# Optimization experiments

Measured on AMD Instinct MI355X. Metric: run time of the kernel, lower is better.

Reference implementation:

```python
import jax, jax.numpy as jnp
import numpy as np

B, S, D, H = 4, 2048, 512, 8

def setup_inputs() -> dict:
    key = jax.random.key(0)
    ks = jax.random.split(key, 6)
    query = jax.random.normal(ks[0], (B, S, D), dtype=jnp.float32)
    value = jax.random.normal(ks[1], (B, S, D), dtype=jnp.float32)
    # causal additive mask, broadcast over heads: [H, S, S]
    causal = jnp.where(jnp.tril(jnp.ones((S, S), dtype=bool)), 0.0, -1e9).astype(jnp.float32)
    mask = jnp.broadcast_to(causal[None, :, :], (H, S, S))
    sd = 1.0 / np.sqrt(D)
    Wq = jax.random.normal(ks[2], (D, D), dtype=jnp.float32) * sd
    Wkv = jax.random.normal(ks[3], (D, 2 * D), dtype=jnp.float32) * sd
    Wo = jax.random.normal(ks[4], (D, D), dtype=jnp.float32) * sd
    normalizer = jnp.asarray(1.0 / np.sqrt(D // H), dtype=jnp.float32)  # 1/sqrt(head_size)
    head_mults = jnp.ones((1, 1, H, 1), dtype=jnp.float32)
    return {"query": query, "value": value, "mask": mask, "Wq": Wq, "Wkv": Wkv,
            "Wo": Wo, "normalizer": normalizer, "head_mults": head_mults}

def reference(query, value, mask, Wq, Wkv, Wo, normalizer, head_mults):
    b, sq, d = query.shape
    h = head_mults.shape[2]
    q = (query @ Wq).reshape(b, sq, h, -1)                 # [b,q,h,hd]
    k, v = jnp.split(value @ Wkv, 2, axis=-1)
    sk = value.shape[1]
    k = k.reshape(b, sk, h, -1)
    v = v.reshape(b, sk, h, -1)
    score = jnp.einsum('bqhd,bkhd->bhqk', q, k) * normalizer
    score = score + mask[None, :, :, :]
    align = jax.nn.softmax(score, axis=-1)
    heads = jnp.einsum('bhqk,bkhd->bqhd', align, v)        # [b,q,h,hd]
    # cross-head normalization (over head axis, ddof=0 like tf.reduce_std)
    mean = jnp.mean(heads, axis=-2, keepdims=True)
    std = jnp.std(heads, axis=-2, keepdims=True)
    heads = (heads - mean) / (std + 0.01)
    heads = heads * head_mults
    out = heads.reshape(b, sq, d) @ Wo
    return out
```

## Files before the change

kernel.cpp:

```cpp
#include <hip/hip_runtime.h>


typedef float  f32x4  __attribute__((ext_vector_type(4)));
typedef __bf16 bf16x8 __attribute__((ext_vector_type(8)));
typedef short  s16x4  __attribute__((ext_vector_type(4)));
typedef unsigned short u16;

#define BS 2048
#define DD 512
#define NH 8
#define NQ (4 * BS * DD)

__device__ __forceinline__ u16 f2bf(float f) {
  union { float f; unsigned u; } v; v.f = f;
  unsigned r = v.u + 0x7fffu + ((v.u >> 16) & 1u);
  return (u16)(r >> 16);
}
__device__ __forceinline__ float bf2f(u16 b) {
  union { unsigned u; float f; } v; v.u = ((unsigned)b) << 16; return v.f;
}

__device__ __forceinline__ void gll16(const u16* g, u16* l) {
  __builtin_amdgcn_global_load_lds((const __attribute__((address_space(1))) void*)g,
                                   (__attribute__((address_space(3))) void*)l, 16, 0, 0);
}

#if defined(__has_builtin)
#if __has_builtin(__builtin_amdgcn_mfma_f32_16x16x16bf16_1k)
#define HAVE_1K 1
#endif
#endif
__device__ __forceinline__ f32x4 mfma_pv(s16x4 a, s16x4 b, f32x4 c) {
#ifdef HAVE_1K
  return __builtin_amdgcn_mfma_f32_16x16x16bf16_1k(a, b, c, 0, 0, 0);
#else
  bf16x8 a8 = {}, b8 = {};
  *(s16x4*)&a8 = a; *(s16x4*)&b8 = b;
  return __builtin_amdgcn_mfma_f32_16x16x32_bf16(a8, b8, c, 0, 0, 0);
#endif
}

__global__ __launch_bounds__(256) void prep(const float* __restrict__ q,
                                            const float* __restrict__ v,
                                            const float* __restrict__ Wq,
                                            const float* __restrict__ Wkv,
                                            const float* __restrict__ Wo,
                                            u16* __restrict__ qb, u16* __restrict__ vb,
                                            u16* __restrict__ WqT, u16* __restrict__ WkvT,
                                            u16* __restrict__ WoT) {
  __shared__ float Ts[64][65];
  const int t = threadIdx.x;
  int bx = blockIdx.x;
  if (bx < 8192) {
    int i = (bx * 256 + t) * 4;
    const float* s; u16* d;
    if (i < NQ) { s = q + i; d = qb + i; }
    else        { s = v + (i - NQ); d = vb + (i - NQ); }
    float4 x = *(const float4*)s;
    ushort4 o; o.x = f2bf(x.x); o.y = f2bf(x.y); o.z = f2bf(x.z); o.w = f2bf(x.w);
    *(ushort4*)d = o;
    return;
  }
  int tb = bx - 8192;
  const float* W; u16* Wt; int N, ntn;
  if (tb < 64)       { W = Wq;  Wt = WqT;  N = 512;  ntn = 8; }
  else if (tb < 192) { W = Wkv; Wt = WkvT; N = 1024; ntn = 16; tb -= 64; }
  else               { W = Wo;  Wt = WoT;  N = 512;  ntn = 8;  tb -= 192; }
  int tk = tb / ntn, tn = tb - tk * ntn;
  int r = t >> 2, c0 = (t & 3) * 16;
  const float* src = &W[(long)(tk * 64 + r) * N + tn * 64 + c0];
#pragma unroll
  for (int j = 0; j < 4; ++j) {
    float4 x = *(const float4*)(src + j * 4);
    Ts[r][c0 + j * 4 + 0] = x.x; Ts[r][c0 + j * 4 + 1] = x.y;
    Ts[r][c0 + j * 4 + 2] = x.z; Ts[r][c0 + j * 4 + 3] = x.w;
  }
  __syncthreads();
  u16* dst = &Wt[(long)(tn * 64 + r) * 512 + tk * 64 + c0];
#pragma unroll
  for (int m = 0; m < 4; ++m) {
    ushort4 o;
    o.x = f2bf(Ts[c0 + m * 4 + 0][r]); o.y = f2bf(Ts[c0 + m * 4 + 1][r]);
    o.z = f2bf(Ts[c0 + m * 4 + 2][r]); o.w = f2bf(Ts[c0 + m * 4 + 3][r]);
    *(ushort4*)(dst + m * 4) = o;
  }
}

__device__ __forceinline__ void gemm_core(const u16* __restrict__ A,
                                          const u16* __restrict__ Bt,
                                          int m0, int n0, int K,
                                          u16* Al, u16* Bl, f32x4 acc[4][4]) {
  const int t = threadIdx.x;
  const int wv = t >> 6, ln = t & 63, qd = ln >> 4, l16 = ln & 15;
  const int rw = (wv & 1) * 64, cw = (wv >> 1) * 64;
  const int sr = wv * 16 + (ln >> 2), sc = (ln & 3) * 8;
  for (int k0 = 0; k0 < K; k0 += 32) {
    __syncthreads();
#pragma unroll
    for (int c = 0; c < 2; ++c) {
      int r = c * 64 + sr;
      gll16(&A[(long)(m0 + r) * K + k0 + sc], &Al[r * 32 + sc]);
      gll16(&Bt[(long)(n0 + r) * K + k0 + sc], &Bl[r * 32 + sc]);
    }
    __syncthreads();
    bf16x8 af[4], bfr[4];
#pragma unroll
    for (int i = 0; i < 4; ++i) af[i] = *(const bf16x8*)&Al[(rw + i * 16 + l16) * 32 + qd * 8];
#pragma unroll
    for (int j = 0; j < 4; ++j) bfr[j] = *(const bf16x8*)&Bl[(cw + j * 16 + l16) * 32 + qd * 8];
#pragma unroll
    for (int i = 0; i < 4; ++i)
#pragma unroll
      for (int j = 0; j < 4; ++j)
        acc[i][j] = __builtin_amdgcn_mfma_f32_16x16x32_bf16(af[i], bfr[j], acc[i][j], 0, 0, 0);
  }
}

__global__ __launch_bounds__(256) void qkv_gemm(const u16* __restrict__ qA,
                                                const u16* __restrict__ vA,
                                                const u16* __restrict__ WqT,
                                                const u16* __restrict__ WkvT,
                                                u16* __restrict__ Qb,
                                                u16* __restrict__ Kb,
                                                u16* __restrict__ Vt) {
  __shared__ __align__(16) u16 Al[128 * 32];
  __shared__ __align__(16) u16 Bl[128 * 32];
  const bool isQ = blockIdx.y < 4;
  const u16* A = isQ ? qA : vA;
  const u16* Bt = isQ ? WqT : WkvT;
  const int n0 = (isQ ? blockIdx.y : blockIdx.y - 4) * 128;
  const int m0 = blockIdx.x * 128;
  f32x4 acc[4][4] = {};
  gemm_core(A, Bt, m0, n0, 512, Al, Bl, acc);
  const int t = threadIdx.x;
  const int wv = t >> 6, ln = t & 63, qd = ln >> 4, l16 = ln & 15;
  const int rw = (wv & 1) * 64, cw = (wv >> 1) * 64;
  if (isQ) {
#pragma unroll
    for (int i = 0; i < 4; ++i)
#pragma unroll
      for (int j = 0; j < 4; ++j) {
        int row = m0 + rw + i * 16 + qd * 4, col = n0 + cw + j * 16 + l16;
#pragma unroll
        for (int r = 0; r < 4; ++r)
          Qb[(long)(row + r) * 512 + col] = f2bf(acc[i][j][r]);
      }
  } else {
#pragma unroll
    for (int j = 0; j < 4; ++j) {
      int col = n0 + cw + j * 16 + l16;
      if (col < 512) {
#pragma unroll
        for (int i = 0; i < 4; ++i) {
          int row = m0 + rw + i * 16 + qd * 4;
#pragma unroll
          for (int r = 0; r < 4; ++r)
            Kb[(long)(row + r) * 512 + col] = f2bf(acc[i][j][r]);
        }
      } else {
        int c2 = col - 512, hh = c2 >> 6, dd = c2 & 63;
#pragma unroll
        for (int i = 0; i < 4; ++i) {
          int sg = m0 + rw + i * 16 + qd * 4;
          int bb = sg >> 11, ss = sg & 2047;
          ushort4 o;
          o.x = f2bf(acc[i][j][0]); o.y = f2bf(acc[i][j][1]);
          o.z = f2bf(acc[i][j][2]); o.w = f2bf(acc[i][j][3]);
          *(ushort4*)&Vt[((long)(bb * 8 + hh) * 64 + dd) * 2048 + ss] = o;
        }
      }
    }
  }
}

__global__ __launch_bounds__(256) void out_gemm(const u16* __restrict__ A,
                                                const u16* __restrict__ Bt,
                                                float* __restrict__ C) {
  __shared__ __align__(16) u16 Al[128 * 32];
  __shared__ __align__(16) u16 Bl[128 * 32];
  const int m0 = blockIdx.x * 128, n0 = blockIdx.y * 128;
  f32x4 acc[4][4] = {};
  gemm_core(A, Bt, m0, n0, 512, Al, Bl, acc);
  const int t = threadIdx.x;
  const int wv = t >> 6, ln = t & 63, qd = ln >> 4, l16 = ln & 15;
  const int rw = (wv & 1) * 64, cw = (wv >> 1) * 64;
#pragma unroll
  for (int i = 0; i < 4; ++i)
#pragma unroll
    for (int j = 0; j < 4; ++j) {
      int row = m0 + rw + i * 16 + qd * 4, col = n0 + cw + j * 16 + l16;
#pragma unroll
      for (int r = 0; r < 4; ++r)
        C[(long)(row + r) * 512 + col] = acc[i][j][r];
    }
}

__global__ __launch_bounds__(256) void attn(const u16* __restrict__ Qb,
                                            const u16* __restrict__ Kb,
                                            const u16* __restrict__ Vt,
                                            u16* __restrict__ heads,
                                            const float* __restrict__ normp) {
  constexpr int ST = 72;
  __shared__ __align__(16) u16 Qs[64 * ST], Ks[64 * ST], Vts[64 * ST];
  const float scale2 = normp[0] * 1.44269504f;
  const int t = threadIdx.x;
  const int wv = t >> 6, ln = t & 63, qd = ln >> 4, l16 = ln & 15;
  const int sr = t >> 2, scg = (t & 3) * 16;
  const int h = blockIdx.y, b = blockIdx.z;
  const int bs0 = b * BS;
  const u16* vtb = Vt + ((long)(b * 8 + h) * 64) * 2048;

  for (int qsel = 0; qsel < 2; ++qsel) {
    const int qt = qsel ? (31 - (int)blockIdx.x) : (int)blockIdx.x;
    __syncthreads();
    {
      const u16* src = &Qb[(long)(bs0 + qt * 64 + sr) * 512 + h * 64 + scg];
      *(bf16x8*)&Qs[sr * ST + scg] = *(const bf16x8*)src;
      *(bf16x8*)&Qs[sr * ST + scg + 8] = *(const bf16x8*)(src + 8);
    }
    bf16x8 kr0, kr1, vr0, vr1;
#define FETCH(KB) do { \
      const u16* kp_ = &Kb[(long)(bs0 + (KB) * 64 + sr) * 512 + h * 64 + scg]; \
      kr0 = *(const bf16x8*)kp_; kr1 = *(const bf16x8*)(kp_ + 8); \
      const u16* vp_ = &vtb[(long)sr * 2048 + (KB) * 64 + scg]; \
      vr0 = *(const bf16x8*)vp_; vr1 = *(const bf16x8*)(vp_ + 8); } while (0)
    FETCH(0);
    float m_i = -1e30f, l_i = 0.f;
    f32x4 o[4] = {};

    for (int kb = 0; kb <= qt; ++kb) {
      __syncthreads();
      *(bf16x8*)&Ks[sr * ST + scg] = kr0;
      *(bf16x8*)&Ks[sr * ST + scg + 8] = kr1;
      *(bf16x8*)&Vts[sr * ST + scg] = vr0;
      *(bf16x8*)&Vts[sr * ST + scg + 8] = vr1;
      __syncthreads();
      if (kb < qt) FETCH(kb + 1);

      f32x4 s[4] = {};
#pragma unroll
      for (int c = 0; c < 2; ++c) {
        bf16x8 bq = *(const bf16x8*)&Qs[(wv * 16 + l16) * ST + c * 32 + qd * 8];
#pragma unroll
        for (int nt = 0; nt < 4; ++nt) {
          bf16x8 ak = *(const bf16x8*)&Ks[(nt * 16 + l16) * ST + c * 32 + qd * 8];
          s[nt] = __builtin_amdgcn_mfma_f32_16x16x32_bf16(ak, bq, s[nt], 0, 0, 0);
        }
      }

      const int limi = (kb == qt) ? (wv * 16 + l16) : 1 << 20;
      float mx = -1e30f;
#pragma unroll
      for (int nt = 0; nt < 4; ++nt)
#pragma unroll
        for (int r = 0; r < 4; ++r) {
          float v = s[nt][r] * scale2;
          if (nt * 16 + qd * 4 + r > limi) v = -1e30f;
          s[nt][r] = v;
          mx = fmaxf(mx, v);
        }
      mx = fmaxf(mx, __shfl_xor(mx, 16));
      mx = fmaxf(mx, __shfl_xor(mx, 32));
      float mn = fmaxf(m_i, mx);
      float al = exp2f(m_i - mn);
      float rs = 0.f;
#pragma unroll
      for (int nt = 0; nt < 4; ++nt)
#pragma unroll
        for (int r = 0; r < 4; ++r) {
          float p = exp2f(s[nt][r] - mn);
          s[nt][r] = p;
          rs += p;
        }
      rs += __shfl_xor(rs, 16);
      rs += __shfl_xor(rs, 32);
      l_i = l_i * al + rs;
      m_i = mn;
#pragma unroll
      for (int n2 = 0; n2 < 4; ++n2) o[n2] *= al;

      s16x4 pf[4];
#pragma unroll
      for (int c2 = 0; c2 < 4; ++c2)
#pragma unroll
        for (int j = 0; j < 4; ++j) pf[c2][j] = (short)f2bf(s[c2][j]);

#pragma unroll
      for (int n2 = 0; n2 < 4; ++n2)
#pragma unroll
        for (int c2 = 0; c2 < 4; ++c2) {
          s16x4 av = *(const s16x4*)&Vts[(n2 * 16 + l16) * ST + c2 * 16 + qd * 4];
          o[n2] = mfma_pv(av, pf[c2], o[n2]);
        }
    }
#undef FETCH

    float inv = 1.f / l_i;
    __syncthreads();
#pragma unroll
    for (int n2 = 0; n2 < 4; ++n2)
#pragma unroll
      for (int r = 0; r < 4; ++r)
        Ks[(wv * 16 + l16) * ST + n2 * 16 + qd * 4 + r] = f2bf(o[n2][r] * inv);
    __syncthreads();
    {
      u16* dst = &heads[(long)(bs0 + qt * 64 + sr) * 512 + h * 64 + scg];
      *(bf16x8*)dst = *(const bf16x8*)&Ks[sr * ST + scg];
      *(bf16x8*)(dst + 8) = *(const bf16x8*)&Ks[sr * ST + scg + 8];
    }
  }
}

__global__ __launch_bounds__(256) void headnorm(const u16* __restrict__ heads,
                                                const float* __restrict__ hm,
                                                u16* __restrict__ outn) {
  int i = blockIdx.x * 256 + threadIdx.x;
  int d = i & 63, bs = i >> 6;
  const u16* p = heads + (long)bs * DD + d;
  float x[NH], mean = 0.f;
#pragma unroll
  for (int h = 0; h < NH; ++h) { x[h] = bf2f(p[h * 64]); mean += x[h]; }
  mean *= 0.125f;
  float var = 0.f;
#pragma unroll
  for (int h = 0; h < NH; ++h) { float dd = x[h] - mean; var += dd * dd; }
  var *= 0.125f;
  float inv = 1.f / (sqrtf(var) + 0.01f);
#pragma unroll
  for (int h = 0; h < NH; ++h)
    outn[(long)bs * DD + h * 64 + d] = f2bf((x[h] - mean) * inv * hm[h]);
}

extern "C" void kernel_launch(void* const* d_in, const int* in_sizes, int n_in,
                              void* d_out, int out_size, void* d_ws, size_t ws_size,
                              hipStream_t stream) {
  const float* query = (const float*)d_in[0];
  const float* value = (const float*)d_in[1];
  const float* Wq    = (const float*)d_in[3];
  const float* Wkv   = (const float*)d_in[4];
  const float* Wo    = (const float*)d_in[5];
  const float* normp = (const float*)d_in[6];
  const float* hmult = (const float*)d_in[7];

  char* ws = (char*)d_ws;
  const size_t MB = 1 << 20;
  u16*   qbf   = (u16*)(ws);
  u16*   vbf   = (u16*)(ws + 8 * MB);
  u16*   WqT   = (u16*)(ws + 16 * MB);
  u16*   WkvT  = (u16*)(ws + 16 * MB + 524288);
  u16*   WoT   = (u16*)(ws + 17 * MB + 524288);
  u16*   Qb    = (u16*)(ws + 18 * MB);
  u16*   Kb    = (u16*)(ws + 26 * MB);
  u16*   Vt    = (u16*)(ws + 34 * MB);
  u16*   heads = (u16*)(ws + 42 * MB);
  u16*   hN    = (u16*)(ws + 50 * MB);

  prep<<<8448, 256, 0, stream>>>(query, value, Wq, Wkv, Wo,
                                 qbf, vbf, WqT, WkvT, WoT);
  qkv_gemm<<<dim3(64, 12), 256, 0, stream>>>(qbf, vbf, WqT, WkvT, Qb, Kb, Vt);
  attn<<<dim3(16, NH, 4), 256, 0, stream>>>(Qb, Kb, Vt, heads, normp);
  headnorm<<<(4 * BS * 64) / 256, 256, 0, stream>>>(heads, hmult, hN);
  out_gemm<<<dim3(64, 4), 256, 0, stream>>>(hN, WoT, (float*)d_out);
}
```

Baseline: 302.9 us.

## Split attention keys across two blocks and merge partials in head-norm kernel

The attention kernel now splits each query tile's causal key range into two halves handled by separate blocks (doubling the grid), writes unnormalized partial outputs plus running max and sum, and the head-norm kernel merges the two partials before normalizing. Each iteration processes 128 keys with 16x16x32 MFMA for PV, Q is held in registers, and the register-prefetch pipeline is removed. This targets low occupancy and the long serial loop for late query tiles, at the cost of extra partial-output traffic and the loss of load/compute overlap.

Result: slower. 309.0 us (+2.0%).

```diff
diff --git a/kernel.cpp b/kernel.cpp
--- a/kernel.cpp
+++ b/kernel.cpp
@@ -23,21 +23,6 @@
 __device__ __forceinline__ void gll16(const u16* g, u16* l) {
   __builtin_amdgcn_global_load_lds((const __attribute__((address_space(1))) void*)g,
                                    (__attribute__((address_space(3))) void*)l, 16, 0, 0);
-}
-
-#if defined(__has_builtin)
-#if __has_builtin(__builtin_amdgcn_mfma_f32_16x16x16bf16_1k)
-#define HAVE_1K 1
-#endif
-#endif
-__device__ __forceinline__ f32x4 mfma_pv(s16x4 a, s16x4 b, f32x4 c) {
-#ifdef HAVE_1K
-  return __builtin_amdgcn_mfma_f32_16x16x16bf16_1k(a, b, c, 0, 0, 0);
-#else
-  bf16x8 a8 = {}, b8 = {};
-  *(s16x4*)&a8 = a; *(s16x4*)&b8 = b;
-  return __builtin_amdgcn_mfma_f32_16x16x32_bf16(a8, b8, c, 0, 0, 0);
-#endif
 }
 
 __global__ __launch_bounds__(256) void prep(const float* __restrict__ q,
@@ -195,77 +180,96 @@
     }
 }
 
-__global__ __launch_bounds__(256) void attn(const u16* __restrict__ Qb,
-                                            const u16* __restrict__ Kb,
-                                            const u16* __restrict__ Vt,
-                                            u16* __restrict__ heads,
-                                            const float* __restrict__ normp) {
-  constexpr int ST = 72;
-  __shared__ __align__(16) u16 Qs[64 * ST], Ks[64 * ST], Vts[64 * ST];
+__global__ __launch_bounds__(256, 4) void attn(const u16* __restrict__ Qb,
+                                               const u16* __restrict__ Kb,
+                                               const u16* __restrict__ Vt,
+                                               u16* __restrict__ Opart,
+                                               float* __restrict__ Ml,
+                                               float* __restrict__ Ll,
+                                               const float* __restrict__ normp) {
+  constexpr int KST = 72;
+  constexpr int VST = 136;
+  __shared__ __align__(16) u16 Ks[128 * KST];
+  __shared__ __align__(16) u16 Vts[64 * VST];
   const float scale2 = normp[0] * 1.44269504f;
   const int t = threadIdx.x;
   const int wv = t >> 6, ln = t & 63, qd = ln >> 4, l16 = ln & 15;
-  const int sr = t >> 2, scg = (t & 3) * 16;
+  const int pairx = blockIdx.x & 15, sp = blockIdx.x >> 4;
   const int h = blockIdx.y, b = blockIdx.z;
   const int bs0 = b * BS;
   const u16* vtb = Vt + ((long)(b * 8 + h) * 64) * 2048;
+  const int krow = t >> 1, kc0 = (t & 1) * 32;
+  const int vrow = t >> 2, vc0 = (t & 3) * 32;
 
   for (int qsel = 0; qsel < 2; ++qsel) {
-    const int qt = qsel ? (31 - (int)blockIdx.x) : (int)blockIdx.x;
-    __syncthreads();
-    {
-      const u16* src = &Qb[(long)(bs0 + qt * 64 + sr) * 512 + h * 64 + scg];
-      *(bf16x8*)&Qs[sr * ST + scg] = *(const bf16x8*)src;
-      *(bf16x8*)&Qs[sr * ST + scg + 8] = *(const bf16x8*)(src + 8);
-    }
-    bf16x8 kr0, kr1, vr0, vr1;
-#define FETCH(KB) do { \
-      const u16* kp_ = &Kb[(long)(bs0 + (KB) * 64 + sr) * 512 + h * 64 + scg]; \
-      kr0 = *(const bf16x8*)kp_; kr1 = *(const bf16x8*)(kp_ + 8); \
-      const u16* vp_ = &vtb[(long)sr * 2048 + (KB) * 64 + scg]; \
-      vr0 = *(const bf16x8*)vp_; vr1 = *(const bf16x8*)(vp_ + 8); } while (0)
-    FETCH(0);
+    const int qt = qsel ? (31 - pairx) : pairx;
+    const int n = qt + 1, n0 = (n + 1) >> 1;
+    const int base = sp ? n0 : 0;
+    const int cnt = sp ? (n - n0) : n0;
+    const int nc = (cnt + 1) >> 1;
+    const int qi = qt * 64 + wv * 16 + l16;
+
+    bf16x8 bq[2];
+#pragma unroll
+    for (int c = 0; c < 2; ++c)
+      bq[c] = *(const bf16x8*)&Qb[(long)(bs0 + qi) * 512 + h * 64 + c * 32 + qd * 8];
+
     float m_i = -1e30f, l_i = 0.f;
     f32x4 o[4] = {};
 
-    for (int kb = 0; kb <= qt; ++kb) {
+    for (int ci = 0; ci < nc; ++ci) {
+      const int ta = base + 2 * ci;
+      const bool has2 = (2 * ci + 1 < cnt);
+      const int tb2 = has2 ? ta + 1 : ta;
       __syncthreads();
-      *(bf16x8*)&Ks[sr * ST + scg] = kr0;
-      *(bf16x8*)&Ks[sr * ST + scg + 8] = kr1;
-      *(bf16x8*)&Vts[sr * ST + scg] = vr0;
-      *(bf16x8*)&Vts[sr * ST + scg + 8] = vr1;
+      {
+        const int tt = (krow < 64) ? ta : tb2;
+        const u16* src = &Kb[(long)(bs0 + tt * 64 + (krow & 63)) * 512 + h * 64 + kc0];
+        u16* dst = &Ks[krow * KST + kc0];
+#pragma unroll
+        for (int j = 0; j < 4; ++j)
+          *(bf16x8*)(dst + j * 8) = *(const bf16x8*)(src + j * 8);
+      }
+      {
+        const int tt = (vc0 < 64) ? ta : tb2;
+        const u16* src = &vtb[(long)vrow * 2048 + tt * 64 + (vc0 & 63)];
+        u16* dst = &Vts[vrow * VST + vc0];
+#pragma unroll
+        for (int j = 0; j < 4; ++j)
+          *(bf16x8*)(dst + j * 8) = *(const bf16x8*)(src + j * 8);
+      }
       __syncthreads();
-      if (kb < qt) FETCH(kb + 1);
-
-      f32x4 s[4] = {};
-#pragma unroll
-      for (int c = 0; c < 2; ++c) {
-        bf16x8 bq = *(const bf16x8*)&Qs[(wv * 16 + l16) * ST + c * 32 + qd * 8];
-#pragma unroll
-        for (int nt = 0; nt < 4; ++nt) {
-          bf16x8 ak = *(const bf16x8*)&Ks[(nt * 16 + l16) * ST + c * 32 + qd * 8];
-          s[nt] = __builtin_amdgcn_mfma_f32_16x16x32_bf16(ak, bq, s[nt], 0, 0, 0);
-        }
-      }
-
-      const int limi = (kb == qt) ? (wv * 16 + l16) : 1 << 20;
+
+      f32x4 s[8] = {};
+#pragma unroll
+      for (int nt = 0; nt < 8; ++nt)
+#pragma unroll
+        for (int c = 0; c < 2; ++c) {
+          bf16x8 ak = *(const bf16x8*)&Ks[(nt * 16 + l16) * KST + c * 32 + qd * 8];
+          s[nt] = __builtin_amdgcn_mfma_f32_16x16x32_bf16(ak, bq[c], s[nt], 0, 0, 0);
+        }
+
       float mx = -1e30f;
 #pragma unroll
-      for (int nt = 0; nt < 4; ++nt)
+      for (int nt = 0; nt < 8; ++nt) {
+        const int tt = (nt < 4) ? ta : tb2;
+        const bool hv = (nt < 4) || has2;
 #pragma unroll
         for (int r = 0; r < 4; ++r) {
+          int key = tt * 64 + ((nt & 3) * 16 + qd * 4 + r);
           float v = s[nt][r] * scale2;
-          if (nt * 16 + qd * 4 + r > limi) v = -1e30f;
+          if (!hv || key > qi) v = -1e30f;
           s[nt][r] = v;
           mx = fmaxf(mx, v);
         }
+      }
       mx = fmaxf(mx, __shfl_xor(mx, 16));
       mx = fmaxf(mx, __shfl_xor(mx, 32));
       float mn = fmaxf(m_i, mx);
       float al = exp2f(m_i - mn);
       float rs = 0.f;
 #pragma unroll
-      for (int nt = 0; nt < 4; ++nt)
+      for (int nt = 0; nt < 8; ++nt)
 #pragma unroll
         for (int r = 0; r < 4; ++r) {
           float p = exp2f(s[nt][r] - mn);
@@ -279,47 +283,66 @@
 #pragma unroll
       for (int n2 = 0; n2 < 4; ++n2) o[n2] *= al;
 
-      s16x4 pf[4];
-#pragma unroll
-      for (int c2 = 0; c2 < 4; ++c2)
-#pragma unroll
-        for (int j = 0; j < 4; ++j) pf[c2][j] = (short)f2bf(s[c2][j]);
-
-#pragma unroll
-      for (int n2 = 0; n2 < 4; ++n2)
-#pragma unroll
-        for (int c2 = 0; c2 < 4; ++c2) {
-          s16x4 av = *(const s16x4*)&Vts[(n2 * 16 + l16) * ST + c2 * 16 + qd * 4];
-          o[n2] = mfma_pv(av, pf[c2], o[n2]);
-        }
-    }
-#undef FETCH
-
-    float inv = 1.f / l_i;
+#pragma unroll
+      for (int c2 = 0; c2 < 4; ++c2) {
+        bf16x8 pb;
+        s16x4* ph = (s16x4*)&pb;
+#pragma unroll
+        for (int j = 0; j < 4; ++j) {
+          ph[0][j] = (short)f2bf(s[c2][j]);
+          ph[1][j] = (short)f2bf(s[4 + c2][j]);
+        }
+#pragma unroll
+        for (int n2 = 0; n2 < 4; ++n2) {
+          bf16x8 av;
+          s16x4* ah = (s16x4*)&av;
+          const u16* vp = &Vts[(n2 * 16 + l16) * VST + c2 * 16 + qd * 4];
+          ah[0] = *(const s16x4*)vp;
+          ah[1] = *(const s16x4*)(vp + 64);
+          o[n2] = __builtin_amdgcn_mfma_f32_16x16x32_bf16(av, pb, o[n2], 0, 0, 0);
+        }
+      }
+    }
+
+    const long mlidx = ((long)((sp * 4 + b) * 8 + h)) * 2048 + qt * 64 + wv * 16 + l16;
+    if (qd == 0) { Ml[mlidx] = m_i; Ll[mlidx] = l_i; }
+
     __syncthreads();
 #pragma unroll
     for (int n2 = 0; n2 < 4; ++n2)
 #pragma unroll
       for (int r = 0; r < 4; ++r)
-        Ks[(wv * 16 + l16) * ST + n2 * 16 + qd * 4 + r] = f2bf(o[n2][r] * inv);
+        Ks[(wv * 16 + l16) * KST + n2 * 16 + qd * 4 + r] = f2bf(o[n2][r]);
     __syncthreads();
     {
-      u16* dst = &heads[(long)(bs0 + qt * 64 + sr) * 512 + h * 64 + scg];
-      *(bf16x8*)dst = *(const bf16x8*)&Ks[sr * ST + scg];
-      *(bf16x8*)(dst + 8) = *(const bf16x8*)&Ks[sr * ST + scg + 8];
-    }
-  }
-}
-
-__global__ __launch_bounds__(256) void headnorm(const u16* __restrict__ heads,
-                                                const float* __restrict__ hm,
-                                                u16* __restrict__ outn) {
+      const int sr = t >> 2, scg = (t & 3) * 16;
+      u16* dst = &Opart[(((long)((sp * 4 + b) * 8 + h)) * 2048 + qt * 64 + sr) * 64 + scg];
+      *(bf16x8*)dst = *(const bf16x8*)&Ks[sr * KST + scg];
+      *(bf16x8*)(dst + 8) = *(const bf16x8*)&Ks[sr * KST + scg + 8];
+    }
+  }
+}
+
+__global__ __launch_bounds__(256) void combine_norm(const u16* __restrict__ Opart,
+                                                    const float* __restrict__ Ml,
+                                                    const float* __restrict__ Ll,
+                                                    const float* __restrict__ hm,
+                                                    u16* __restrict__ outn) {
   int i = blockIdx.x * 256 + threadIdx.x;
-  int d = i & 63, bs = i >> 6;
-  const u16* p = heads + (long)bs * DD + d;
+  int d = i & 63, s = (i >> 6) & 2047, b = i >> 17;
   float x[NH], mean = 0.f;
 #pragma unroll
-  for (int h = 0; h < NH; ++h) { x[h] = bf2f(p[h * 64]); mean += x[h]; }
+  for (int h = 0; h < NH; ++h) {
+    long i0 = ((long)(b * 8 + h)) * 2048 + s;
+    long i1 = ((long)((4 + b) * 8 + h)) * 2048 + s;
+    float m0 = Ml[i0], l0 = Ll[i0], m1 = Ml[i1], l1 = Ll[i1];
+    float m = fmaxf(m0, m1);
+    float a0 = exp2f(m0 - m), a1 = exp2f(m1 - m);
+    float l = l0 * a0 + l1 * a1;
+    float o0 = bf2f(Opart[i0 * 64 + d]), o1 = bf2f(Opart[i1 * 64 + d]);
+    x[h] = (o0 * a0 + o1 * a1) / l;
+    mean += x[h];
+  }
   mean *= 0.125f;
   float var = 0.f;
 #pragma unroll
@@ -328,7 +351,7 @@
   float inv = 1.f / (sqrtf(var) + 0.01f);
 #pragma unroll
   for (int h = 0; h < NH; ++h)
-    outn[(long)bs * DD + h * 64 + d] = f2bf((x[h] - mean) * inv * hm[h]);
+    outn[((long)(b * 2048 + s)) * 512 + h * 64 + d] = f2bf((x[h] - mean) * inv * hm[h]);
 }
 
 extern "C" void kernel_launch(void* const* d_in, const int* in_sizes, int n_in,
@@ -352,13 +375,15 @@
   u16*   Qb    = (u16*)(ws + 18 * MB);
   u16*   Kb    = (u16*)(ws + 26 * MB);
   u16*   Vt    = (u16*)(ws + 34 * MB);
-  u16*   heads = (u16*)(ws + 42 * MB);
-  u16*   hN    = (u16*)(ws + 50 * MB);
+  u16*   Opart = (u16*)(ws + 42 * MB);
+  float* Ml    = (float*)(ws + 58 * MB);
+  float* Ll    = (float*)(ws + 58 * MB + 524288);
+  u16*   hN    = (u16*)(ws + 59 * MB);
 
   prep<<<8448, 256, 0, stream>>>(query, value, Wq, Wkv, Wo,
                                  qbf, vbf, WqT, WkvT, WoT);
   qkv_gemm<<<dim3(64, 12), 256, 0, stream>>>(qbf, vbf, WqT, WkvT, Qb, Kb, Vt);
-  attn<<<dim3(16, NH, 4), 256, 0, stream>>>(Qb, Kb, Vt, heads, normp);
-  headnorm<<<(4 * BS * 64) / 256, 256, 0, stream>>>(heads, hmult, hN);
+  attn<<<dim3(32, NH, 4), 256, 0, stream>>>(Qb, Kb, Vt, Opart, Ml, Ll, normp);
+  combine_norm<<<(4 * BS * 64) / 256, 256, 0, stream>>>(Opart, Ml, Ll, hmult, hN);
   out_gemm<<<dim3(64, 4), 256, 0, stream>>>(hN, WoT, (float*)d_out);
 }
```

## Double-buffer K/V LDS tiles, keep Q in registers, use K=32 MFMA for PV

Applied to the files above, without the earlier changes.

The attention kernel now ping-pongs two LDS buffers for K and V, which removes one of the two block barriers per key tile. Q fragments are loaded straight from global memory into registers instead of being staged through LDS. The PV product packs two 16-key chunks into a single 16x16x32 bf16 MFMA, halving the number of MFMA issues. A min-waves-per-EU launch bound of 4 is added, which adds register pressure and doubles LDS use for K/V.

New measurement: 293.9 us. -3.0%, faster.

```diff
diff --git a/kernel.cpp b/kernel.cpp
--- a/kernel.cpp
+++ b/kernel.cpp
@@ -23,21 +23,6 @@
 __device__ __forceinline__ void gll16(const u16* g, u16* l) {
   __builtin_amdgcn_global_load_lds((const __attribute__((address_space(1))) void*)g,
                                    (__attribute__((address_space(3))) void*)l, 16, 0, 0);
-}
-
-#if defined(__has_builtin)
-#if __has_builtin(__builtin_amdgcn_mfma_f32_16x16x16bf16_1k)
-#define HAVE_1K 1
-#endif
-#endif
-__device__ __forceinline__ f32x4 mfma_pv(s16x4 a, s16x4 b, f32x4 c) {
-#ifdef HAVE_1K
-  return __builtin_amdgcn_mfma_f32_16x16x16bf16_1k(a, b, c, 0, 0, 0);
-#else
-  bf16x8 a8 = {}, b8 = {};
-  *(s16x4*)&a8 = a; *(s16x4*)&b8 = b;
-  return __builtin_amdgcn_mfma_f32_16x16x32_bf16(a8, b8, c, 0, 0, 0);
-#endif
 }
 
 __global__ __launch_bounds__(256) void prep(const float* __restrict__ q,
@@ -195,13 +180,14 @@
     }
 }
 
-__global__ __launch_bounds__(256) void attn(const u16* __restrict__ Qb,
-                                            const u16* __restrict__ Kb,
-                                            const u16* __restrict__ Vt,
-                                            u16* __restrict__ heads,
-                                            const float* __restrict__ normp) {
+__global__ __launch_bounds__(256, 4) void attn(const u16* __restrict__ Qb,
+                                               const u16* __restrict__ Kb,
+                                               const u16* __restrict__ Vt,
+                                               u16* __restrict__ heads,
+                                               const float* __restrict__ normp) {
   constexpr int ST = 72;
-  __shared__ __align__(16) u16 Qs[64 * ST], Ks[64 * ST], Vts[64 * ST];
+  __shared__ __align__(16) u16 Ks[2][64 * ST];
+  __shared__ __align__(16) u16 Vts[2][64 * ST];
   const float scale2 = normp[0] * 1.44269504f;
   const int t = threadIdx.x;
   const int wv = t >> 6, ln = t & 63, qd = ln >> 4, l16 = ln & 15;
@@ -212,12 +198,13 @@
 
   for (int qsel = 0; qsel < 2; ++qsel) {
     const int qt = qsel ? (31 - (int)blockIdx.x) : (int)blockIdx.x;
-    __syncthreads();
-    {
-      const u16* src = &Qb[(long)(bs0 + qt * 64 + sr) * 512 + h * 64 + scg];
-      *(bf16x8*)&Qs[sr * ST + scg] = *(const bf16x8*)src;
-      *(bf16x8*)&Qs[sr * ST + scg + 8] = *(const bf16x8*)(src + 8);
-    }
+    const int qi = qt * 64 + wv * 16 + l16;
+
+    bf16x8 bq[2];
+#pragma unroll
+    for (int c = 0; c < 2; ++c)
+      bq[c] = *(const bf16x8*)&Qb[(long)(bs0 + qi) * 512 + h * 64 + c * 32 + qd * 8];
+
     bf16x8 kr0, kr1, vr0, vr1;
 #define FETCH(KB) do { \
       const u16* kp_ = &Kb[(long)(bs0 + (KB) * 64 + sr) * 512 + h * 64 + scg]; \
@@ -229,24 +216,22 @@
     f32x4 o[4] = {};
 
     for (int kb = 0; kb <= qt; ++kb) {
-      __syncthreads();
-      *(bf16x8*)&Ks[sr * ST + scg] = kr0;
-      *(bf16x8*)&Ks[sr * ST + scg + 8] = kr1;
-      *(bf16x8*)&Vts[sr * ST + scg] = vr0;
-      *(bf16x8*)&Vts[sr * ST + scg + 8] = vr1;
+      const int buf = kb & 1;
+      *(bf16x8*)&Ks[buf][sr * ST + scg] = kr0;
+      *(bf16x8*)&Ks[buf][sr * ST + scg + 8] = kr1;
+      *(bf16x8*)&Vts[buf][sr * ST + scg] = vr0;
+      *(bf16x8*)&Vts[buf][sr * ST + scg + 8] = vr1;
       __syncthreads();
       if (kb < qt) FETCH(kb + 1);
 
       f32x4 s[4] = {};
 #pragma unroll
-      for (int c = 0; c < 2; ++c) {
-        bf16x8 bq = *(const bf16x8*)&Qs[(wv * 16 + l16) * ST + c * 32 + qd * 8];
+      for (int c = 0; c < 2; ++c)
 #pragma unroll
         for (int nt = 0; nt < 4; ++nt) {
-          bf16x8 ak = *(const bf16x8*)&Ks[(nt * 16 + l16) * ST + c * 32 + qd * 8];
-          s[nt] = __builtin_amdgcn_mfma_f32_16x16x32_bf16(ak, bq, s[nt], 0, 0, 0);
-        }
-      }
+          bf16x8 ak = *(const bf16x8*)&Ks[buf][(nt * 16 + l16) * ST + c * 32 + qd * 8];
+          s[nt] = __builtin_amdgcn_mfma_f32_16x16x32_bf16(ak, bq[c], s[nt], 0, 0, 0);
+        }
 
       const int limi = (kb == qt) ? (wv * 16 + l16) : 1 << 20;
       float mx = -1e30f;
@@ -279,19 +264,25 @@
 #pragma unroll
       for (int n2 = 0; n2 < 4; ++n2) o[n2] *= al;
 
-      s16x4 pf[4];
-#pragma unroll
-      for (int c2 = 0; c2 < 4; ++c2)
-#pragma unroll
-        for (int j = 0; j < 4; ++j) pf[c2][j] = (short)f2bf(s[c2][j]);
-
-#pragma unroll
-      for (int n2 = 0; n2 < 4; ++n2)
-#pragma unroll
-        for (int c2 = 0; c2 < 4; ++c2) {
-          s16x4 av = *(const s16x4*)&Vts[(n2 * 16 + l16) * ST + c2 * 16 + qd * 4];
-          o[n2] = mfma_pv(av, pf[c2], o[n2]);
-        }
+#pragma unroll
+      for (int cp = 0; cp < 2; ++cp) {
+        bf16x8 pb;
+        s16x4* ph = (s16x4*)&pb;
+#pragma unroll
+        for (int j = 0; j < 4; ++j) {
+          ph[0][j] = (short)f2bf(s[cp * 2][j]);
+          ph[1][j] = (short)f2bf(s[cp * 2 + 1][j]);
+        }
+#pragma unroll
+        for (int n2 = 0; n2 < 4; ++n2) {
+          bf16x8 av;
+          s16x4* ah = (s16x4*)&av;
+          const u16* vp = &Vts[buf][(n2 * 16 + l16) * ST + cp * 32 + qd * 4];
+          ah[0] = *(const s16x4*)vp;
+          ah[1] = *(const s16x4*)(vp + 16);
+          o[n2] = __builtin_amdgcn_mfma_f32_16x16x32_bf16(av, pb, o[n2], 0, 0, 0);
+        }
+      }
     }
 #undef FETCH
 
@@ -301,13 +292,14 @@
     for (int n2 = 0; n2 < 4; ++n2)
 #pragma unroll
       for (int r = 0; r < 4; ++r)
-        Ks[(wv * 16 + l16) * ST + n2 * 16 + qd * 4 + r] = f2bf(o[n2][r] * inv);
+        Ks[0][(wv * 16 + l16) * ST + n2 * 16 + qd * 4 + r] = f2bf(o[n2][r] * inv);
     __syncthreads();
     {
       u16* dst = &heads[(long)(bs0 + qt * 64 + sr) * 512 + h * 64 + scg];
-      *(bf16x8*)dst = *(const bf16x8*)&Ks[sr * ST + scg];
-      *(bf16x8*)(dst + 8) = *(const bf16x8*)&Ks[sr * ST + scg + 8];
-    }
+      *(bf16x8*)dst = *(const bf16x8*)&Ks[0][sr * ST + scg];
+      *(bf16x8*)(dst + 8) = *(const bf16x8*)&Ks[0][sr * ST + scg + 8];
+    }
+    __syncthreads();
   }
 }
 
```
